# Kernel optimization log

Hardware: AMD Instinct MI355X
Metric: run time of the kernel (lower is better)

Reference implementation:

```python
import jax, jax.numpy as jnp
import numpy as np

N = 50000   # nodes
E = 800000  # edges
F = 256     # input features
H = 256     # hidden units
L = 128     # n_labels
EPS = 1e-5


def setup_inputs():
    key = jax.random.key(0)
    ks = jax.random.split(key, 17)
    s = 0.05
    return {
        "features": jax.random.normal(ks[0], (N, F), jnp.float32),
        "edge_vals": jax.random.uniform(ks[1], (E,), jnp.float32),
        "W1": jax.random.normal(ks[2], (F, H), jnp.float32) * s,
        "db1": jax.random.normal(ks[3], (H,), jnp.float32) * s,
        "b1": jax.random.normal(ks[4], (H,), jnp.float32) * s,
        "g1": jax.random.uniform(ks[5], (H,), jnp.float32, 0.5, 1.5),
        "be1": jax.random.normal(ks[6], (H,), jnp.float32) * s,
        "W2": jax.random.normal(ks[7], (H, H), jnp.float32) * s,
        "b2": jax.random.normal(ks[8], (H,), jnp.float32) * s,
        "g2": jax.random.uniform(ks[9], (H,), jnp.float32, 0.5, 1.5),
        "be2": jax.random.normal(ks[10], (H,), jnp.float32) * s,
        "Wf": jax.random.normal(ks[11], (H, L), jnp.float32) * s,
        "bf": jax.random.normal(ks[12], (L,), jnp.float32) * s,
        "edge_rows": jax.random.randint(ks[13], (E,), 0, N, jnp.int32),
        "edge_cols": jax.random.randint(ks[14], (E,), 0, N, jnp.int32),
        "idx": jax.random.randint(ks[15], (N // 2,), 0, N, jnp.int32),
    }


def _spmm(edge_vals, rows, cols, x):
    # out[i] = sum_{(i,j) in E} A[i,j] * x[j]  (COO sparse @ dense)
    return jax.ops.segment_sum(edge_vals[:, None] * x[cols], rows, num_segments=N)


def _bn(x, gamma, beta):
    # training-mode BatchNormalization: batch (population) stats over nodes
    m = jnp.mean(x, axis=0)
    v = jnp.var(x, axis=0)
    return (x - m) * jax.lax.rsqrt(v + EPS) * gamma + beta


def reference(features, edge_vals, W1, db1, b1, g1, be1, W2, b2, g2, be2, Wf, bf,
              edge_rows, edge_cols, idx):
    # layer 1 (Dense has bias only for l == 0)
    h = features @ W1 + db1
    h = _spmm(edge_vals, edge_rows, edge_cols, h) + b1
    h = jax.nn.relu(_bn(h, g1, be1))
    # layer 2 (no dense bias)
    h = h @ W2
    h = _spmm(edge_vals, edge_rows, edge_cols, h) + b2
    h = jax.nn.relu(_bn(h, g2, be2))
    # dropout = identity (deterministic baseline); final dense head
    out = h @ Wf + bf
    return out[idx]
```

## Files before the change

kernel.cpp:

```cpp
#include <hip/hip_runtime.h>
#include <stdint.h>

#define NN 50000
#define EE 800000
#define FF 256
#define HH 256
#define LL 128
#define SBLK 512

typedef __bf16 bf16x8 __attribute__((ext_vector_type(8)));
typedef float  f32x4  __attribute__((ext_vector_type(4)));

typedef __attribute__((address_space(1))) unsigned int uint_as1;
typedef __attribute__((address_space(3))) unsigned int uint_as3;

__device__ __forceinline__ unsigned short f2bf(float f) {
  union { float f; unsigned int u; } v; v.f = f;
  unsigned int u = v.u;
  u += 0x7FFFu + ((u >> 16) & 1u);
  return (unsigned short)(u >> 16);
}

__device__ __forceinline__ float bf2f(unsigned short u) {
  union { unsigned int u; float f; } v;
  v.u = ((unsigned int)u) << 16;
  return v.f;
}

__device__ __forceinline__ f32x4 bf4_to_f32(ushort4 u) {
  f32x4 r;
  r.x = bf2f(u.x); r.y = bf2f(u.y); r.z = bf2f(u.z); r.w = bf2f(u.w);
  return r;
}

__device__ __forceinline__ void gload_lds16(const void* g, void* l) {
  __builtin_amdgcn_global_load_lds((const uint_as1*)g, (uint_as3*)l, 16, 0, 0);
}

__global__ __launch_bounds__(256) void k_casts(const float* __restrict__ features,
                                               unsigned short* __restrict__ Xb,
                                               const float* __restrict__ W1,
                                               unsigned short* __restrict__ W1t,
                                               const float* __restrict__ W2,
                                               unsigned short* __restrict__ W2t,
                                               const float* __restrict__ Wf,
                                               unsigned short* __restrict__ Wft) {
  int b = blockIdx.x, t = threadIdx.x;
  if (b < 12500) {
    int i = b * 256 + t;
    f32x4 x = ((const f32x4*)features)[i];
    ushort4 o;
    o.x = f2bf(x.x); o.y = f2bf(x.y); o.z = f2bf(x.z); o.w = f2bf(x.w);
    ((ushort4*)Xb)[i] = o;
  } else if (b < 13012) {
    const float* in = (b < 12756) ? W1 : W2;
    unsigned short* out = (b < 12756) ? W1t : W2t;
    int i = ((b < 12756) ? (b - 12500) : (b - 12756)) * 256 + t;
    int n = i >> 8, k = i & 255;
    out[i] = f2bf(in[k * HH + n]);
  } else {
    int i = (b - 13012) * 256 + t;
    int n = i >> 8, k = i & 255;
    Wft[i] = f2bf(Wf[k * LL + n]);
  }
}

__global__ __launch_bounds__(256) void k_hist(const int* __restrict__ rows,
                                              int* __restrict__ cnt, int E) {
  int i = blockIdx.x * 256 + threadIdx.x;
  if (i < E) atomicAdd(&cnt[rows[i]], 1);
}

__global__ __launch_bounds__(256) void k_alloc(const int* __restrict__ cnt,
                                               int* __restrict__ cursor,
                                               int* __restrict__ total, int n) {
  int i = blockIdx.x * 256 + threadIdx.x;
  int lane = threadIdx.x & 63;
  int c = (i < n) ? cnt[i] : 0;
  int incl = c;
#pragma unroll
  for (int off = 1; off < 64; off <<= 1) {
    int v = __shfl_up(incl, off, 64);
    if (lane >= off) incl += v;
  }
  int excl = incl - c;
  int wtot = __shfl(incl, 63, 64);
  int base = 0;
  if (lane == 0) base = atomicAdd(total, wtot);
  base = __shfl(base, 0, 64);
  if (i < n) cursor[i] = base + excl;
}

__global__ __launch_bounds__(256) void k_fill(const int* __restrict__ rows,
                                              const int* __restrict__ cols,
                                              const float* __restrict__ vals,
                                              int* __restrict__ cursor,
                                              unsigned int* __restrict__ csr, int E) {
  int i = blockIdx.x * 256 + threadIdx.x;
  if (i < E) {
    int p = atomicAdd(&cursor[rows[i]], 1);
    csr[p] = ((unsigned int)cols[i] << 16) | (unsigned int)f2bf(vals[i]);
  }
}

__global__ __launch_bounds__(256) void k_spmm(const unsigned short* __restrict__ X,
                                              const int* __restrict__ endp,
                                              const int* __restrict__ cnt,
                                              const unsigned int* __restrict__ csr,
                                              unsigned short* __restrict__ Y, int n) {
  int row = blockIdx.x * 4 + (threadIdx.x >> 6);
  int lane = threadIdx.x & 63;
  if (row >= n) return;
  int e = endp[row];
  int s = e - cnt[row];
  f32x4 a0 = {0.f, 0.f, 0.f, 0.f};
  f32x4 a1 = a0, a2 = a0, a3 = a0, a4 = a0, a5 = a0, a6 = a0, a7 = a0;
  int p = s;
  int e8 = s + ((e - s) & ~7);
  for (; p < e8; p += 8) {
    unsigned int c0 = csr[p + 0], c1 = csr[p + 1], c2 = csr[p + 2], c3 = csr[p + 3];
    unsigned int c4 = csr[p + 4], c5 = csr[p + 5], c6 = csr[p + 6], c7 = csr[p + 7];
    ushort4 x0 = ((const ushort4*)(X + (size_t)(c0 >> 16) * HH))[lane];
    ushort4 x1 = ((const ushort4*)(X + (size_t)(c1 >> 16) * HH))[lane];
    ushort4 x2 = ((const ushort4*)(X + (size_t)(c2 >> 16) * HH))[lane];
    ushort4 x3 = ((const ushort4*)(X + (size_t)(c3 >> 16) * HH))[lane];
    ushort4 x4 = ((const ushort4*)(X + (size_t)(c4 >> 16) * HH))[lane];
    ushort4 x5 = ((const ushort4*)(X + (size_t)(c5 >> 16) * HH))[lane];
    ushort4 x6 = ((const ushort4*)(X + (size_t)(c6 >> 16) * HH))[lane];
    ushort4 x7 = ((const ushort4*)(X + (size_t)(c7 >> 16) * HH))[lane];
    a0 += bf2f((unsigned short)c0) * bf4_to_f32(x0);
    a1 += bf2f((unsigned short)c1) * bf4_to_f32(x1);
    a2 += bf2f((unsigned short)c2) * bf4_to_f32(x2);
    a3 += bf2f((unsigned short)c3) * bf4_to_f32(x3);
    a4 += bf2f((unsigned short)c4) * bf4_to_f32(x4);
    a5 += bf2f((unsigned short)c5) * bf4_to_f32(x5);
    a6 += bf2f((unsigned short)c6) * bf4_to_f32(x6);
    a7 += bf2f((unsigned short)c7) * bf4_to_f32(x7);
  }
  for (; p < e; ++p) {
    unsigned int c0 = csr[p];
    ushort4 x0 = ((const ushort4*)(X + (size_t)(c0 >> 16) * HH))[lane];
    a0 += bf2f((unsigned short)c0) * bf4_to_f32(x0);
  }
  f32x4 a = ((a0 + a1) + (a2 + a3)) + ((a4 + a5) + (a6 + a7));
  ushort4 o;
  o.x = f2bf(a.x); o.y = f2bf(a.y); o.z = f2bf(a.z); o.w = f2bf(a.w);
  ((ushort4*)(Y + (size_t)row * HH))[lane] = o;
}

__global__ __launch_bounds__(256) void k_bnstats(const unsigned short* __restrict__ X,
                                                 float* __restrict__ part, int n) {
  __shared__ float red[4][64][9];
  const int w = threadIdx.x >> 6, l = threadIdx.x & 63;
  f32x4 s = {0.f, 0.f, 0.f, 0.f}, s2 = {0.f, 0.f, 0.f, 0.f};
  for (int r = blockIdx.x * 4 + w; r < n; r += gridDim.x * 4) {
    f32x4 v = bf4_to_f32(((const ushort4*)(X + (size_t)r * HH))[l]);
    s += v;
    s2 += v * v;
  }
#pragma unroll
  for (int j = 0; j < 4; ++j) { red[w][l][j] = s[j]; red[w][l][4 + j] = s2[j]; }
  __syncthreads();
  if (threadIdx.x < 64) {
    int ll = threadIdx.x;
#pragma unroll
    for (int j = 0; j < 8; ++j) {
      float v = red[0][ll][j] + red[1][ll][j] + red[2][ll][j] + red[3][ll][j];
      int c = ll * 4 + (j & 3);
      part[((j < 4) ? 0 : (SBLK * 256)) + blockIdx.x * 256 + c] = v;
    }
  }
}

__global__ __launch_bounds__(256) void k_bnred(const float* __restrict__ part,
                                               float* __restrict__ sums) {
  int c = threadIdx.x;
  const float* p = part + blockIdx.x * (SBLK * 256);
  float s0 = 0.f, s1 = 0.f, s2 = 0.f, s3 = 0.f;
  for (int b = 0; b < SBLK; b += 4) {
    s0 += p[(b + 0) * 256 + c];
    s1 += p[(b + 1) * 256 + c];
    s2 += p[(b + 2) * 256 + c];
    s3 += p[(b + 3) * 256 + c];
  }
  sums[blockIdx.x * HH + c] = (s0 + s1) + (s2 + s3);
}

__global__ __launch_bounds__(256) void k_bnrc(const unsigned short* __restrict__ X,
                                              const float* __restrict__ sums,
                                              const float* __restrict__ g,
                                              const float* __restrict__ be,
                                              unsigned short* __restrict__ out, int n4) {
  __shared__ float sc[HH], sh[HH];
  int t = threadIdx.x;
  {
    float inv = 1.f / (float)NN;
    float mean = sums[t] * inv;
    float var = sums[HH + t] * inv - mean * mean;
    float s = g[t] * rsqrtf(var + 1e-5f);
    sc[t] = s;
    sh[t] = be[t] - mean * s;
  }
  __syncthreads();
  for (int i = blockIdx.x * 256 + t; i < n4; i += gridDim.x * 256) {
    f32x4 x = bf4_to_f32(((const ushort4*)X)[i]);
    int c0 = (i * 4) & (HH - 1);
    ushort4 o;
    o.x = f2bf(fmaxf(x.x * sc[c0 + 0] + sh[c0 + 0], 0.f));
    o.y = f2bf(fmaxf(x.y * sc[c0 + 1] + sh[c0 + 1], 0.f));
    o.z = f2bf(fmaxf(x.z * sc[c0 + 2] + sh[c0 + 2], 0.f));
    o.w = f2bf(fmaxf(x.w * sc[c0 + 3] + sh[c0 + 3], 0.f));
    ((ushort4*)out)[i] = o;
  }
}

template <int OUTB>
__global__ __launch_bounds__(256, 2) void k_gemm(const unsigned short* __restrict__ A,
                                                 const unsigned short* __restrict__ Bt,
                                                 const float* __restrict__ bias,
                                                 void* __restrict__ Cv,
                                                 int M, int K, int Nn,
                                                 const int* __restrict__ gather) {
  __shared__ unsigned short lA[128 * 32];
  __shared__ unsigned short lB[128 * 32];
  const int tid = threadIdx.x;
  const int wave = tid >> 6, lane = tid & 63;
  const int m0 = blockIdx.x * 128, n0 = blockIdx.y * 128;
  const int wm = (wave >> 1) * 64, wn = (wave & 1) * 64;
  const int lhi = lane >> 4, llo = lane & 15;

  const int srow = wave * 16 + (lane >> 2);
  const int scol = (lane & 3) * 8;
  int ar0 = m0 + srow, ar1 = m0 + 64 + srow;
  ar0 = ar0 < M ? ar0 : 0;
  ar1 = ar1 < M ? ar1 : 0;
  if (gather) { ar0 = gather[ar0]; ar1 = gather[ar1]; }
  const unsigned short* pA0 = A + (size_t)ar0 * K + scol;
  const unsigned short* pA1 = A + (size_t)ar1 * K + scol;
  const unsigned short* pB0 = Bt + (size_t)(n0 + srow) * K + scol;
  const unsigned short* pB1 = Bt + (size_t)(n0 + 64 + srow) * K + scol;
  unsigned short* dA0 = lA + (wave * 16) * 32;
  unsigned short* dA1 = lA + (64 + wave * 16) * 32;
  unsigned short* dB0 = lB + (wave * 16) * 32;
  unsigned short* dB1 = lB + (64 + wave * 16) * 32;

  f32x4 zero = {0.f, 0.f, 0.f, 0.f};
  f32x4 acc[4][4];
#pragma unroll
  for (int i = 0; i < 4; ++i)
#pragma unroll
    for (int j = 0; j < 4; ++j) acc[i][j] = zero;

  for (int k0 = 0; k0 < K; k0 += 32) {
    gload_lds16(pA0 + k0, dA0);
    gload_lds16(pA1 + k0, dA1);
    gload_lds16(pB0 + k0, dB0);
    gload_lds16(pB1 + k0, dB1);
    __syncthreads();
    bf16x8 af[4], bfv[4];
#pragma unroll
    for (int mt = 0; mt < 4; ++mt)
      af[mt] = *(const bf16x8*)(lA + (wm + mt * 16 + llo) * 32 + lhi * 8);
#pragma unroll
    for (int nt = 0; nt < 4; ++nt)
      bfv[nt] = *(const bf16x8*)(lB + (wn + nt * 16 + llo) * 32 + lhi * 8);
#pragma unroll
    for (int mt = 0; mt < 4; ++mt)
#pragma unroll
      for (int nt = 0; nt < 4; ++nt)
        acc[mt][nt] = __builtin_amdgcn_mfma_f32_16x16x32_bf16(af[mt], bfv[nt], acc[mt][nt], 0, 0, 0);
    __syncthreads();
  }

#pragma unroll
  for (int nt = 0; nt < 4; ++nt) {
    int cn = n0 + wn + nt * 16 + llo;
    float bv = bias ? bias[cn] : 0.f;
#pragma unroll
    for (int mt = 0; mt < 4; ++mt) {
      int cm0 = m0 + wm + mt * 16 + lhi * 4;
#pragma unroll
      for (int r = 0; r < 4; ++r) {
        int cm = cm0 + r;
        if (cm < M) {
          float v = acc[mt][nt][r] + bv;
          if (OUTB)
            ((unsigned short*)Cv)[(size_t)cm * Nn + cn] = f2bf(v);
          else
            ((float*)Cv)[(size_t)cm * Nn + cn] = v;
        }
      }
    }
  }
}

extern "C" void kernel_launch(void* const* d_in, const int* in_sizes, int n_in,
                              void* d_out, int out_size, void* d_ws, size_t ws_size,
                              hipStream_t stream) {
  const float* features = (const float*)d_in[0];
  const float* edge_vals = (const float*)d_in[1];
  const float* W1 = (const float*)d_in[2];
  const float* db1 = (const float*)d_in[3];
  const float* g1 = (const float*)d_in[5];
  const float* be1 = (const float*)d_in[6];
  const float* W2 = (const float*)d_in[7];
  const float* g2 = (const float*)d_in[9];
  const float* be2 = (const float*)d_in[10];
  const float* Wf = (const float*)d_in[11];
  const float* bfb = (const float*)d_in[12];
  const int* erows = (const int*)d_in[13];
  const int* ecols = (const int*)d_in[14];
  const int* idx = (const int*)d_in[15];
  const int M3 = in_sizes[15];
  (void)n_in; (void)out_size; (void)ws_size;

  char* ws = (char*)d_ws;
  size_t off = 0;
  auto alloc = [&](size_t bytes) -> void* {
    void* p = (void*)(ws + off);
    off += (bytes + 255) & ~(size_t)255;
    return p;
  };
  unsigned short* Xb = (unsigned short*)alloc((size_t)NN * HH * 2);
  unsigned short* Ab = (unsigned short*)alloc((size_t)NN * HH * 2);
  unsigned short* Yb = (unsigned short*)alloc((size_t)NN * HH * 2);
  unsigned short* W1t = (unsigned short*)alloc((size_t)FF * HH * 2);
  unsigned short* W2t = (unsigned short*)alloc((size_t)HH * HH * 2);
  unsigned short* Wft = (unsigned short*)alloc((size_t)HH * LL * 2);
  int* cursor = (int*)alloc((size_t)NN * 4);
  int* cnt = (int*)alloc((size_t)NN * 4);
  unsigned int* csr = (unsigned int*)alloc((size_t)EE * 4);
  float* part = (float*)alloc((size_t)2 * SBLK * 256 * 4);
  float* stats = (float*)alloc(4 * HH * 4 + 256);
  float* sums1 = stats;
  float* sums2 = stats + 2 * HH;
  int* total = (int*)(stats + 4 * HH);

  hipMemsetAsync(cnt, 0, (size_t)NN * 4, stream);
  hipMemsetAsync(total, 0, 256, stream);

  k_casts<<<13140, 256, 0, stream>>>(features, Xb, W1, W1t, W2, W2t, Wf, Wft);

  k_hist<<<(EE + 255) / 256, 256, 0, stream>>>(erows, cnt, EE);
  k_alloc<<<(NN + 255) / 256, 256, 0, stream>>>(cnt, cursor, total, NN);
  k_fill<<<(EE + 255) / 256, 256, 0, stream>>>(erows, ecols, edge_vals, cursor, csr, EE);

  k_gemm<1><<<dim3((NN + 127) / 128, HH / 128), 256, 0, stream>>>(Xb, W1t, db1, Ab, NN, FF, HH, nullptr);
  k_spmm<<<(NN + 3) / 4, 256, 0, stream>>>(Ab, cursor, cnt, csr, Yb, NN);
  k_bnstats<<<SBLK, 256, 0, stream>>>(Yb, part, NN);
  k_bnred<<<2, 256, 0, stream>>>(part, sums1);
  k_bnrc<<<2048, 256, 0, stream>>>(Yb, sums1, g1, be1, Xb, NN * HH / 4);

  k_gemm<1><<<dim3((NN + 127) / 128, HH / 128), 256, 0, stream>>>(Xb, W2t, nullptr, Ab, NN, HH, HH, nullptr);
  k_spmm<<<(NN + 3) / 4, 256, 0, stream>>>(Ab, cursor, cnt, csr, Yb, NN);
  k_bnstats<<<SBLK, 256, 0, stream>>>(Yb, part, NN);
  k_bnred<<<2, 256, 0, stream>>>(part, sums2);
  k_bnrc<<<2048, 256, 0, stream>>>(Yb, sums2, g2, be2, Xb, NN * HH / 4);

  k_gemm<0><<<dim3((M3 + 127) / 128, LL / 128), 256, 0, stream>>>(Xb, Wft, bfb, d_out, M3, HH, LL, idx);
}
```

Before: 463.1 us.

## Tile weight transposes, fold memsets into cast kernel, deepen GEMM K-step, parallelize BN reduce

The cast kernel now transposes weights through an LDS tile for coalesced reads, and it zeroes the histogram counters and stats buffer itself, so the two memset calls go away. The GEMM loads a 64-wide K slice per sync instead of 32, halving the number of barriers. The BN partial reduce is split across 16 blocks that accumulate with atomics, using half as many stats blocks. The SpMM unroll drops from 8 to 4 edges, which frees registers but leaves fewer gathers in flight.

```diff
diff --git a/kernel.cpp b/kernel.cpp
--- a/kernel.cpp
+++ b/kernel.cpp
@@ -6,7 +6,7 @@
 #define FF 256
 #define HH 256
 #define LL 128
-#define SBLK 512
+#define SBLK 256
 
 typedef __bf16 bf16x8 __attribute__((ext_vector_type(8)));
 typedef float  f32x4  __attribute__((ext_vector_type(4)));
@@ -44,7 +44,10 @@
                                                const float* __restrict__ W2,
                                                unsigned short* __restrict__ W2t,
                                                const float* __restrict__ Wf,
-                                               unsigned short* __restrict__ Wft) {
+                                               unsigned short* __restrict__ Wft,
+                                               int* __restrict__ cnt,
+                                               int* __restrict__ statz) {
+  __shared__ float tl[64 * 65];
   int b = blockIdx.x, t = threadIdx.x;
   if (b < 12500) {
     int i = b * 256 + t;
@@ -52,16 +55,44 @@
     ushort4 o;
     o.x = f2bf(x.x); o.y = f2bf(x.y); o.z = f2bf(x.z); o.w = f2bf(x.w);
     ((ushort4*)Xb)[i] = o;
-  } else if (b < 13012) {
-    const float* in = (b < 12756) ? W1 : W2;
-    unsigned short* out = (b < 12756) ? W1t : W2t;
-    int i = ((b < 12756) ? (b - 12500) : (b - 12756)) * 256 + t;
-    int n = i >> 8, k = i & 255;
-    out[i] = f2bf(in[k * HH + n]);
+  } else if (b < 12540) {
+    const float* in;
+    unsigned short* out;
+    int Nin, k0, n0;
+    if (b < 12516) {
+      in = W1; out = W1t; Nin = HH;
+      int tt = b - 12500; k0 = (tt >> 2) * 64; n0 = (tt & 3) * 64;
+    } else if (b < 12532) {
+      in = W2; out = W2t; Nin = HH;
+      int tt = b - 12516; k0 = (tt >> 2) * 64; n0 = (tt & 3) * 64;
+    } else {
+      in = Wf; out = Wft; Nin = LL;
+      int tt = b - 12532; k0 = (tt >> 1) * 64; n0 = (tt & 1) * 64;
+    }
+#pragma unroll
+    for (int j = 0; j < 16; ++j) {
+      int idx = j * 256 + t;
+      int r = idx >> 6, c = idx & 63;
+      tl[r * 65 + c] = in[(size_t)(k0 + r) * Nin + n0 + c];
+    }
+    __syncthreads();
+#pragma unroll
+    for (int j = 0; j < 16; ++j) {
+      int idx = j * 256 + t;
+      int r = idx >> 6, c = idx & 63;
+      out[(size_t)(n0 + r) * HH + k0 + c] = f2bf(tl[c * 65 + r]);
+    }
+  } else if (b < 12589) {
+    int base = (b - 12540) * 1024 + t * 4;
+    if (base + 3 < NN) {
+      int4 z = {0, 0, 0, 0};
+      *(int4*)(cnt + base) = z;
+    } else {
+      for (int j = 0; j < 4; ++j)
+        if (base + j < NN) cnt[base + j] = 0;
+    }
   } else {
-    int i = (b - 13012) * 256 + t;
-    int n = i >> 8, k = i & 255;
-    Wft[i] = f2bf(Wf[k * LL + n]);
+    for (int i = t; i < 4 * HH + 64; i += 256) statz[i] = 0;
   }
 }
 
@@ -114,35 +145,26 @@
   int e = endp[row];
   int s = e - cnt[row];
   f32x4 a0 = {0.f, 0.f, 0.f, 0.f};
-  f32x4 a1 = a0, a2 = a0, a3 = a0, a4 = a0, a5 = a0, a6 = a0, a7 = a0;
+  f32x4 a1 = a0, a2 = a0, a3 = a0;
   int p = s;
-  int e8 = s + ((e - s) & ~7);
-  for (; p < e8; p += 8) {
+  int e4 = s + ((e - s) & ~3);
+  for (; p < e4; p += 4) {
     unsigned int c0 = csr[p + 0], c1 = csr[p + 1], c2 = csr[p + 2], c3 = csr[p + 3];
-    unsigned int c4 = csr[p + 4], c5 = csr[p + 5], c6 = csr[p + 6], c7 = csr[p + 7];
     ushort4 x0 = ((const ushort4*)(X + (size_t)(c0 >> 16) * HH))[lane];
     ushort4 x1 = ((const ushort4*)(X + (size_t)(c1 >> 16) * HH))[lane];
     ushort4 x2 = ((const ushort4*)(X + (size_t)(c2 >> 16) * HH))[lane];
     ushort4 x3 = ((const ushort4*)(X + (size_t)(c3 >> 16) * HH))[lane];
-    ushort4 x4 = ((const ushort4*)(X + (size_t)(c4 >> 16) * HH))[lane];
-    ushort4 x5 = ((const ushort4*)(X + (size_t)(c5 >> 16) * HH))[lane];
-    ushort4 x6 = ((const ushort4*)(X + (size_t)(c6 >> 16) * HH))[lane];
-    ushort4 x7 = ((const ushort4*)(X + (size_t)(c7 >> 16) * HH))[lane];
     a0 += bf2f((unsigned short)c0) * bf4_to_f32(x0);
     a1 += bf2f((unsigned short)c1) * bf4_to_f32(x1);
     a2 += bf2f((unsigned short)c2) * bf4_to_f32(x2);
     a3 += bf2f((unsigned short)c3) * bf4_to_f32(x3);
-    a4 += bf2f((unsigned short)c4) * bf4_to_f32(x4);
-    a5 += bf2f((unsigned short)c5) * bf4_to_f32(x5);
-    a6 += bf2f((unsigned short)c6) * bf4_to_f32(x6);
-    a7 += bf2f((unsigned short)c7) * bf4_to_f32(x7);
   }
   for (; p < e; ++p) {
     unsigned int c0 = csr[p];
     ushort4 x0 = ((const ushort4*)(X + (size_t)(c0 >> 16) * HH))[lane];
     a0 += bf2f((unsigned short)c0) * bf4_to_f32(x0);
   }
-  f32x4 a = ((a0 + a1) + (a2 + a3)) + ((a4 + a5) + (a6 + a7));
+  f32x4 a = (a0 + a1) + (a2 + a3);
   ushort4 o;
   o.x = f2bf(a.x); o.y = f2bf(a.y); o.z = f2bf(a.z); o.w = f2bf(a.w);
   ((ushort4*)(Y + (size_t)row * HH))[lane] = o;
@@ -175,15 +197,16 @@
 __global__ __launch_bounds__(256) void k_bnred(const float* __restrict__ part,
                                                float* __restrict__ sums) {
   int c = threadIdx.x;
-  const float* p = part + blockIdx.x * (SBLK * 256);
+  int stat = blockIdx.x >> 3, chunk = blockIdx.x & 7;
+  const float* p = part + stat * (SBLK * 256) + chunk * 32 * 256;
   float s0 = 0.f, s1 = 0.f, s2 = 0.f, s3 = 0.f;
-  for (int b = 0; b < SBLK; b += 4) {
+  for (int b = 0; b < 32; b += 4) {
     s0 += p[(b + 0) * 256 + c];
     s1 += p[(b + 1) * 256 + c];
     s2 += p[(b + 2) * 256 + c];
     s3 += p[(b + 3) * 256 + c];
   }
-  sums[blockIdx.x * HH + c] = (s0 + s1) + (s2 + s3);
+  atomicAdd(&sums[stat * HH + c], (s0 + s1) + (s2 + s3));
 }
 
 __global__ __launch_bounds__(256) void k_bnrc(const unsigned short* __restrict__ X,
@@ -221,28 +244,26 @@
                                                  void* __restrict__ Cv,
                                                  int M, int K, int Nn,
                                                  const int* __restrict__ gather) {
-  __shared__ unsigned short lA[128 * 32];
-  __shared__ unsigned short lB[128 * 32];
+  __shared__ unsigned short lA[128 * 64];
+  __shared__ unsigned short lB[128 * 64];
   const int tid = threadIdx.x;
   const int wave = tid >> 6, lane = tid & 63;
   const int m0 = blockIdx.x * 128, n0 = blockIdx.y * 128;
   const int wm = (wave >> 1) * 64, wn = (wave & 1) * 64;
   const int lhi = lane >> 4, llo = lane & 15;
 
-  const int srow = wave * 16 + (lane >> 2);
-  const int scol = (lane & 3) * 8;
-  int ar0 = m0 + srow, ar1 = m0 + 64 + srow;
-  ar0 = ar0 < M ? ar0 : 0;
-  ar1 = ar1 < M ? ar1 : 0;
-  if (gather) { ar0 = gather[ar0]; ar1 = gather[ar1]; }
-  const unsigned short* pA0 = A + (size_t)ar0 * K + scol;
-  const unsigned short* pA1 = A + (size_t)ar1 * K + scol;
-  const unsigned short* pB0 = Bt + (size_t)(n0 + srow) * K + scol;
-  const unsigned short* pB1 = Bt + (size_t)(n0 + 64 + srow) * K + scol;
-  unsigned short* dA0 = lA + (wave * 16) * 32;
-  unsigned short* dA1 = lA + (64 + wave * 16) * 32;
-  unsigned short* dB0 = lB + (wave * 16) * 32;
-  unsigned short* dB1 = lB + (64 + wave * 16) * 32;
+  const int srow = lane >> 3;
+  const int scol = (lane & 7) * 8;
+  const unsigned short *pA[4], *pB[4];
+#pragma unroll
+  for (int j = 0; j < 4; ++j) {
+    int base = (wave * 4 + j) * 8 + srow;
+    int ar = m0 + base;
+    ar = ar < M ? ar : 0;
+    if (gather) ar = gather[ar];
+    pA[j] = A + (size_t)ar * K + scol;
+    pB[j] = Bt + (size_t)(n0 + base) * K + scol;
+  }
 
   f32x4 zero = {0.f, 0.f, 0.f, 0.f};
   f32x4 acc[4][4];
@@ -251,24 +272,30 @@
 #pragma unroll
     for (int j = 0; j < 4; ++j) acc[i][j] = zero;
 
-  for (int k0 = 0; k0 < K; k0 += 32) {
-    gload_lds16(pA0 + k0, dA0);
-    gload_lds16(pA1 + k0, dA1);
-    gload_lds16(pB0 + k0, dB0);
-    gload_lds16(pB1 + k0, dB1);
+  for (int k0 = 0; k0 < K; k0 += 64) {
+#pragma unroll
+    for (int j = 0; j < 4; ++j) {
+      gload_lds16(pA[j] + k0, lA + (wave * 4 + j) * 8 * 64);
+      gload_lds16(pB[j] + k0, lB + (wave * 4 + j) * 8 * 64);
+    }
     __syncthreads();
-    bf16x8 af[4], bfv[4];
-#pragma unroll
-    for (int mt = 0; mt < 4; ++mt)
-      af[mt] = *(const bf16x8*)(lA + (wm + mt * 16 + llo) * 32 + lhi * 8);
-#pragma unroll
-    for (int nt = 0; nt < 4; ++nt)
-      bfv[nt] = *(const bf16x8*)(lB + (wn + nt * 16 + llo) * 32 + lhi * 8);
-#pragma unroll
-    for (int mt = 0; mt < 4; ++mt)
+    bf16x8 af[2][4], bfv[2][4];
+#pragma unroll
+    for (int ks = 0; ks < 2; ++ks) {
+#pragma unroll
+      for (int mt = 0; mt < 4; ++mt)
+        af[ks][mt] = *(const bf16x8*)(lA + (wm + mt * 16 + llo) * 64 + ks * 32 + lhi * 8);
 #pragma unroll
       for (int nt = 0; nt < 4; ++nt)
-        acc[mt][nt] = __builtin_amdgcn_mfma_f32_16x16x32_bf16(af[mt], bfv[nt], acc[mt][nt], 0, 0, 0);
+        bfv[ks][nt] = *(const bf16x8*)(lB + (wn + nt * 16 + llo) * 64 + ks * 32 + lhi * 8);
+    }
+#pragma unroll
+    for (int ks = 0; ks < 2; ++ks)
+#pragma unroll
+      for (int mt = 0; mt < 4; ++mt)
+#pragma unroll
+        for (int nt = 0; nt < 4; ++nt)
+          acc[mt][nt] = __builtin_amdgcn_mfma_f32_16x16x32_bf16(af[ks][mt], bfv[ks][nt], acc[mt][nt], 0, 0, 0);
     __syncthreads();
   }
 
@@ -336,10 +363,8 @@
   float* sums2 = stats + 2 * HH;
   int* total = (int*)(stats + 4 * HH);
 
-  hipMemsetAsync(cnt, 0, (size_t)NN * 4, stream);
-  hipMemsetAsync(total, 0, 256, stream);
-
-  k_casts<<<13140, 256, 0, stream>>>(features, Xb, W1, W1t, W2, W2t, Wf, Wft);
+  k_casts<<<12590, 256, 0, stream>>>(features, Xb, W1, W1t, W2, W2t, Wf, Wft,
+                                     cnt, (int*)stats);
 
   k_hist<<<(EE + 255) / 256, 256, 0, stream>>>(erows, cnt, EE);
   k_alloc<<<(NN + 255) / 256, 256, 0, stream>>>(cnt, cursor, total, NN);
@@ -348,13 +373,13 @@
   k_gemm<1><<<dim3((NN + 127) / 128, HH / 128), 256, 0, stream>>>(Xb, W1t, db1, Ab, NN, FF, HH, nullptr);
   k_spmm<<<(NN + 3) / 4, 256, 0, stream>>>(Ab, cursor, cnt, csr, Yb, NN);
   k_bnstats<<<SBLK, 256, 0, stream>>>(Yb, part, NN);
-  k_bnred<<<2, 256, 0, stream>>>(part, sums1);
+  k_bnred<<<16, 256, 0, stream>>>(part, sums1);
   k_bnrc<<<2048, 256, 0, stream>>>(Yb, sums1, g1, be1, Xb, NN * HH / 4);
 
   k_gemm<1><<<dim3((NN + 127) / 128, HH / 128), 256, 0, stream>>>(Xb, W2t, nullptr, Ab, NN, HH, HH, nullptr);
   k_spmm<<<(NN + 3) / 4, 256, 0, stream>>>(Ab, cursor, cnt, csr, Yb, NN);
   k_bnstats<<<SBLK, 256, 0, stream>>>(Yb, part, NN);
-  k_bnred<<<2, 256, 0, stream>>>(part, sums2);
+  k_bnred<<<16, 256, 0, stream>>>(part, sums2);
   k_bnrc<<<2048, 256, 0, stream>>>(Yb, sums2, g2, be2, Xb, NN * HH / 4);
 
   k_gemm<0><<<dim3((M3 + 127) / 128, LL / 128), 256, 0, stream>>>(Xb, Wft, bfb, d_out, M3, HH, LL, idx);
```

After: 455.4 us. Within noise of the previous version (-1.6%).
